# Kernel optimization log

Hardware: AMD Instinct MI355X
Metric: run time of the kernel (lower is better)

The kernel has to match this reference:

```python
import jax, jax.numpy as jnp
import numpy as np

N_OBJ, N_SR, N_V, N_F = 8192, 4096, 4100, 4096
EPS = 1e-8


def setup_inputs() -> dict:
    key = jax.random.key(0)
    k1, k2, k3, k4, k5 = jax.random.split(key, 5)
    obj_points = jax.random.normal(k1, (N_OBJ, 3), jnp.float32)
    sr_points = 0.5 * jax.random.normal(k2, (N_SR, 3), jnp.float32)
    hand_verts = 0.5 * jax.random.normal(k3, (N_V, 3), jnp.float32)
    face_normals = jax.random.normal(k4, (N_F, 3), jnp.float32)
    hand_faces = jax.random.randint(k5, (N_F, 3), 0, N_V)
    return dict(obj_points=obj_points, sr_points=sr_points,
                hand_verts=hand_verts, face_normals=face_normals,
                hand_faces=hand_faces)


def reference(obj_points, sr_points, hand_verts, face_normals, hand_faces):
    # --- get_NN: brute-force nearest hand point for every object point ---
    d2 = (jnp.sum(obj_points**2, -1)[:, None]
          + jnp.sum(sr_points**2, -1)[None, :]
          - 2.0 * obj_points @ sr_points.T)          # [N, M] squared dists
    nn_idx = jnp.argmin(d2, axis=1)                   # [N]
    trg_pts = sr_points[nn_idx]                       # batched_index_select -> [N,3]
    D = trg_pts - obj_points                          # ray directions [N,3]

    # --- ray-triangle intersection (plane test + 3 edge half-plane tests) ---
    # All [F,N,3] intermediates are avoided via triple-product expansion:
    # every quantity reduces to einsums of per-face [F,3] with per-ray [N,3].
    tri = hand_verts[hand_faces]                      # [F,3,3]
    v0, v1, v2 = tri[:, 0], tri[:, 1], tri[:, 2]
    n = face_normals                                  # [F,3]

    denom = jnp.einsum('fk,nk->fn', n, D)             # D . n   [F,N]
    num = jnp.sum(v0 * n, -1)[:, None] - jnp.einsum('fk,nk->fn', n, obj_points)
    dmask = jnp.abs(denom) > EPS
    t = num / jnp.where(dmask, denom, 1.0)            # plane hit parameter [F,N]

    def edge_sign(va, vb):
        # ((vb-va) x (P-va)) . n  with  P = O + t*D, expanded bilinearly
        c = jnp.cross(n, vb - va)                     # [F,3]
        base = (jnp.einsum('fk,nk->fn', c, obj_points)
                - jnp.sum(va * c, -1)[:, None])
        return base + t * jnp.einsum('fk,nk->fn', c, D)

    inside = ((edge_sign(v0, v1) >= 0)
              & (edge_sign(v1, v2) >= 0)
              & (edge_sign(v2, v0) >= 0))
    hit = inside & dmask & (t > EPS)                  # [F,N]

    hit_number = jnp.sum(hit.astype(jnp.int32), axis=0)   # per ray [N]
    interior = (hit_number % 2) != 0                        # odd parity -> inside

    diff = trg_pts - obj_points
    pen_dist = jnp.sqrt(jnp.sum(diff**2 * interior[:, None].astype(diff.dtype)) + 1e-12)

    # --- contact_map_of_m_to_n(obj_points, sr_points) ---
    nn_dist = jnp.sqrt(jnp.maximum(jnp.min(d2, axis=1), 0.0))
    cmap = 1.0 - 2.0 * (jax.nn.sigmoid(100.0 * nn_dist) - 0.5)

    return pen_dist, cmap
```

## Files before the change

### kernel.cpp

```cpp
#include <hip/hip_runtime.h>
#include <math.h>

#define N_OBJ 8192
#define N_SR  4096
#define N_F   4096
#define EPSF  1e-8f

typedef float v2f __attribute__((ext_vector_type(2)));
static __device__ __forceinline__ v2f sp(float x) { v2f r; r.x = x; r.y = x; return r; }
static __device__ __forceinline__ v2f vfma(v2f a, v2f b, v2f c) { return __builtin_elementwise_fma(a, b, c); }
static __device__ __forceinline__ v2f vmin2(v2f a, v2f b) { return __builtin_elementwise_min(a, b); }

__global__ void __launch_bounds__(256) nn_all(const float* __restrict__ obj,
                                              const float* __restrict__ sr,
                                              const float* __restrict__ hv,
                                              const float* __restrict__ fn,
                                              const int* __restrict__ hf,
                                              float* __restrict__ out,
                                              float4* __restrict__ Dws,
                                              int* __restrict__ hits,
                                              float4* __restrict__ F) {
    __shared__ float sx[N_SR], sy[N_SR], sz[N_SR];
    __shared__ float2 red[4][32];
    const int tid = threadIdx.x, b = blockIdx.x;

#pragma unroll
    for (int it = 0; it < 16; ++it) {
        int idx = it * 256 + tid;
        sx[idx] = sr[3 * idx];
        sy[idx] = sr[3 * idx + 1];
        sz[idx] = sr[3 * idx + 2];
    }
    if (tid < 32) hits[b * 32 + tid] = 0;
    if (tid < 16) {
        const int f = b * 16 + tid;
        const int i0 = hf[3*f], i1 = hf[3*f+1], i2 = hf[3*f+2];
        const float v0x = hv[3*i0], v0y = hv[3*i0+1], v0z = hv[3*i0+2];
        const float v1x = hv[3*i1], v1y = hv[3*i1+1], v1z = hv[3*i1+2];
        const float v2x = hv[3*i2], v2y = hv[3*i2+1], v2z = hv[3*i2+2];
        const float nx = fn[3*f], ny = fn[3*f+1], nz = fn[3*f+2];
        F[4*f+0] = make_float4(nx, ny, nz, v0x*nx + v0y*ny + v0z*nz);
        {
            float ex = v1x-v0x, ey = v1y-v0y, ez = v1z-v0z;
            float cx = ny*ez-nz*ey, cy = nz*ex-nx*ez, cz = nx*ey-ny*ex;
            F[4*f+1] = make_float4(cx, cy, cz, v0x*cx + v0y*cy + v0z*cz);
        }
        {
            float ex = v2x-v1x, ey = v2y-v1y, ez = v2z-v1z;
            float cx = ny*ez-nz*ey, cy = nz*ex-nx*ez, cz = nx*ey-ny*ex;
            F[4*f+2] = make_float4(cx, cy, cz, v1x*cx + v1y*cy + v1z*cz);
        }
        {
            float ex = v0x-v2x, ey = v0y-v2y, ez = v0z-v2z;
            float cx = ny*ez-nz*ey, cy = nz*ex-nx*ez, cz = nx*ey-ny*ex;
            F[4*f+3] = make_float4(cx, cy, cz, v2x*cx + v2y*cy + v2z*cz);
        }
    }
    __syncthreads();

    const int w = tid >> 6, lane = tid & 63;
    const int pp = lane >> 3, sl = lane & 7;
    const int s = w * 8 + sl;
    const int pbase = b * 32 + pp * 4;

    float ox[4], oy[4], oz[4];
#pragma unroll
    for (int k = 0; k < 4; ++k) {
        int p = pbase + k;
        ox[k] = obj[3*p]; oy[k] = obj[3*p+1]; oz[k] = obj[3*p+2];
    }
    float bd[4]; int bj[4];
#pragma unroll
    for (int k = 0; k < 4; ++k) { bd[k] = INFINITY; bj[k] = 0; }

#pragma unroll 4
    for (int j = 0; j < 128; ++j) {
        int e = j * 32 + s;
        float vx = sx[e], vy = sy[e], vz = sz[e];
#pragma unroll
        for (int k = 0; k < 4; ++k) {
            float dx = vx - ox[k], dy = vy - oy[k], dz = vz - oz[k];
            float d2 = fmaf(dx, dx, fmaf(dy, dy, dz * dz));
            if (d2 < bd[k]) { bd[k] = d2; bj[k] = j; }
        }
    }
    int bi[4];
#pragma unroll
    for (int k = 0; k < 4; ++k) bi[k] = bj[k] * 32 + s;
#pragma unroll
    for (int off = 4; off; off >>= 1) {
#pragma unroll
        for (int k = 0; k < 4; ++k) {
            float d = __shfl_down(bd[k], off, 8);
            int   i = __shfl_down(bi[k], off, 8);
            if (d < bd[k] || (d == bd[k] && i < bi[k])) { bd[k] = d; bi[k] = i; }
        }
    }
    if (sl == 0) {
#pragma unroll
        for (int k = 0; k < 4; ++k)
            red[w][pp * 4 + k] = make_float2(bd[k], __int_as_float(bi[k]));
    }
    __syncthreads();
    if (tid < 32) {
        float2 e0 = red[0][tid];
        float bdf = e0.x; int bif = __float_as_int(e0.y);
#pragma unroll
        for (int w2 = 1; w2 < 4; ++w2) {
            float2 e2 = red[w2][tid];
            float d = e2.x; int i = __float_as_int(e2.y);
            if (d < bdf || (d == bdf && i < bif)) { bdf = d; bif = i; }
        }
        int p = b * 32 + tid;
        float pox = obj[3*p], poy = obj[3*p+1], poz = obj[3*p+2];
        float dx = sx[bif] - pox, dy = sy[bif] - poy, dz = sz[bif] - poz;
        Dws[p] = make_float4(dx, dy, dz, dx*dx + dy*dy + dz*dz);
        float nn = sqrtf(fmaxf(bdf, 0.f));
        float sig = 1.f / (1.f + expf(-100.f * nn));
        out[1 + p] = 1.f - 2.f * (sig - 0.5f);
    }
}

#define RFC 64
__global__ void __launch_bounds__(256) ray_count(const float* __restrict__ obj,
                                                 const float4* __restrict__ Dws,
                                                 const float4* __restrict__ F,
                                                 int* __restrict__ hits) {
    __shared__ float4 sF[RFC * 4];
    const int tid = threadIdx.x;
    const int pg = blockIdx.x & 3, fc = blockIdx.x >> 2;
    {
        const float* Ff = (const float*)(F + (size_t)fc * RFC * 4);
        float* sf = (float*)sF;
#pragma unroll
        for (int i = 0; i < RFC * 16 / 256; ++i)
            sf[i * 256 + tid] = Ff[i * 256 + tid];
    }
    __syncthreads();

    v2f px[4], py[4], pz[4], qx[4], qy[4], qz[4];
    int cnt[8];
#pragma unroll
    for (int g = 0; g < 4; ++g) {
#pragma unroll
        for (int h = 0; h < 2; ++h) {
            int p = pg * 2048 + (g * 2 + h) * 256 + tid;
            px[g][h] = obj[3*p]; py[g][h] = obj[3*p+1]; pz[g][h] = obj[3*p+2];
            float4 D = Dws[p];
            qx[g][h] = D.x; qy[g][h] = D.y; qz[g][h] = D.z;
            cnt[g * 2 + h] = 0;
        }
    }

#pragma unroll 2
    for (int f = 0; f < RFC; ++f) {
        const float4 Fn = sF[4*f+0];
        const float4 C1 = sF[4*f+1];
        const float4 C2 = sF[4*f+2];
        const float4 C3 = sF[4*f+3];
#pragma unroll
        for (int g = 0; g < 4; ++g) {
            v2f denom = vfma(sp(Fn.z), qz[g], vfma(sp(Fn.y), qy[g], sp(Fn.x) * qx[g]));
            v2f num   = sp(Fn.w) - vfma(sp(Fn.z), pz[g], vfma(sp(Fn.y), py[g], sp(Fn.x) * px[g]));
            v2f dn = __builtin_elementwise_abs(denom);
            v2f nm = __builtin_elementwise_copysign(num, num * denom);
            v2f wx = vfma(px[g], dn, nm * qx[g]);
            v2f wy = vfma(py[g], dn, nm * qy[g]);
            v2f wz = vfma(pz[g], dn, nm * qz[g]);
            v2f q1 = vfma(sp(-C1.w), dn, vfma(sp(C1.z), wz, vfma(sp(C1.y), wy, sp(C1.x) * wx)));
            v2f q2 = vfma(sp(-C2.w), dn, vfma(sp(C2.z), wz, vfma(sp(C2.y), wy, sp(C2.x) * wx)));
            v2f q3 = vfma(sp(-C3.w), dn, vfma(sp(C3.z), wz, vfma(sp(C3.y), wy, sp(C3.x) * wx)));
            v2f mm = vmin2(q1, vmin2(q2, q3));
            mm = vmin2(mm, vfma(sp(-EPSF), dn, nm));
            mm = vmin2(mm, dn - sp(EPSF));
            cnt[g * 2 + 0] += (mm[0] >= 0.f) ? 1 : 0;
            cnt[g * 2 + 1] += (mm[1] >= 0.f) ? 1 : 0;
        }
    }
#pragma unroll
    for (int g = 0; g < 4; ++g) {
        atomicAdd(&hits[pg * 2048 + (g * 2 + 0) * 256 + tid], cnt[g * 2 + 0]);
        atomicAdd(&hits[pg * 2048 + (g * 2 + 1) * 256 + tid], cnt[g * 2 + 1]);
    }
}

__global__ void __launch_bounds__(256) finalize(const float4* __restrict__ Dws,
                                                const int* __restrict__ hits,
                                                float* __restrict__ out) {
    __shared__ float wsum[4];
    const int tid = threadIdx.x;
    float s = 0.f;
#pragma unroll 8
    for (int k = tid; k < N_OBJ; k += 256) {
        if (hits[k] & 1) s += Dws[k].w;
    }
#pragma unroll
    for (int off = 32; off > 0; off >>= 1) s += __shfl_down(s, off);
    if ((tid & 63) == 0) wsum[tid >> 6] = s;
    __syncthreads();
    if (tid == 0) {
        out[0] = sqrtf(wsum[0] + wsum[1] + wsum[2] + wsum[3] + 1e-12f);
    }
}

extern "C" void kernel_launch(void* const* d_in, const int* in_sizes, int n_in,
                              void* d_out, int out_size, void* d_ws, size_t ws_size,
                              hipStream_t stream) {
    const float* obj = (const float*)d_in[0];
    const float* sr  = (const float*)d_in[1];
    const float* hv  = (const float*)d_in[2];
    const float* fn  = (const float*)d_in[3];
    const int*   hf  = (const int*)d_in[4];
    float* out = (float*)d_out;

    char* ws = (char*)d_ws;
    float4* Dws  = (float4*)(ws + 0);
    int*    hits = (int*)  (ws + 131072);
    float4* F    = (float4*)(ws + 163840);

    nn_all<<<N_OBJ / 32, 256, 0, stream>>>(obj, sr, hv, fn, hf, out, Dws, hits, F);
    ray_count<<<256, 256, 0, stream>>>(obj, Dws, F, hits);
    finalize<<<1, 256, 0, stream>>>(Dws, hits, out);
}
```

Baseline: 120.4 us.

## Rework NN search with norm expansion, fuse finalize into ray kernel, rebalance grids

The nearest-neighbour kernel now precomputes squared norms of the hand points into packed shared-memory arrays. It computes distances as |s|^2 - 2 o·s with two-wide vector FMAs and reduces across a full wavefront instead of 8-lane groups plus a shared-memory stage, and it uses 512 blocks of 16 points. The ray kernel uses smaller face chunks over 512 blocks, issues its point loads before the face staging, and folds the final parity sum into the last block via an atomic completion counter, which drops the third launch. The expanded-distance form can change argmin tie and rounding behaviour relative to the direct difference form, and the last-block pattern relies on fences and atomics.

```diff
diff --git a/kernel.cpp b/kernel.cpp
--- a/kernel.cpp
+++ b/kernel.cpp
@@ -19,21 +19,27 @@
                                               float* __restrict__ out,
                                               float4* __restrict__ Dws,
                                               int* __restrict__ hits,
-                                              float4* __restrict__ F) {
-    __shared__ float sx[N_SR], sy[N_SR], sz[N_SR];
-    __shared__ float2 red[4][32];
+                                              float4* __restrict__ F,
+                                              int* __restrict__ done) {
+    __shared__ float4 pXY[N_SR / 2];
+    __shared__ float4 pZS[N_SR / 2];
     const int tid = threadIdx.x, b = blockIdx.x;
 
-#pragma unroll
-    for (int it = 0; it < 16; ++it) {
-        int idx = it * 256 + tid;
-        sx[idx] = sr[3 * idx];
-        sy[idx] = sr[3 * idx + 1];
-        sz[idx] = sr[3 * idx + 2];
-    }
-    if (tid < 32) hits[b * 32 + tid] = 0;
-    if (tid < 16) {
-        const int f = b * 16 + tid;
+    const float2* sr2 = (const float2*)sr;
+#pragma unroll
+    for (int i = 0; i < 8; ++i) {
+        int e = i * 256 + tid;
+        float2 A = sr2[3 * e], B = sr2[3 * e + 1], C = sr2[3 * e + 2];
+        float x0 = A.x, y0 = A.y, z0 = B.x, x1 = B.y, y1 = C.x, z1 = C.y;
+        float s0 = fmaf(x0, x0, fmaf(y0, y0, z0 * z0));
+        float s1 = fmaf(x1, x1, fmaf(y1, y1, z1 * z1));
+        pXY[e] = make_float4(x0, x1, y0, y1);
+        pZS[e] = make_float4(z0, z1, s0, s1);
+    }
+    if (tid < 16) hits[b * 16 + tid] = 0;
+    if (b == 0 && tid == 0) done[0] = 0;
+    if (tid < 8) {
+        const int f = b * 8 + tid;
         const int i0 = hf[3*f], i1 = hf[3*f+1], i2 = hf[3*f+2];
         const float v0x = hv[3*i0], v0y = hv[3*i0+1], v0z = hv[3*i0+2];
         const float v1x = hv[3*i1], v1y = hv[3*i1+1], v1z = hv[3*i1+2];
@@ -59,84 +65,80 @@
     __syncthreads();
 
     const int w = tid >> 6, lane = tid & 63;
-    const int pp = lane >> 3, sl = lane & 7;
-    const int s = w * 8 + sl;
-    const int pbase = b * 32 + pp * 4;
-
-    float ox[4], oy[4], oz[4];
+    const int pbase = b * 16 + w * 4;
+
+    float ox[4], oy[4], oz[4], aa[4];
 #pragma unroll
     for (int k = 0; k < 4; ++k) {
         int p = pbase + k;
         ox[k] = obj[3*p]; oy[k] = obj[3*p+1]; oz[k] = obj[3*p+2];
-    }
-    float bd[4]; int bj[4];
-#pragma unroll
-    for (int k = 0; k < 4; ++k) { bd[k] = INFINITY; bj[k] = 0; }
-
+        aa[k] = fmaf(ox[k], ox[k], fmaf(oy[k], oy[k], oz[k] * oz[k]));
+    }
+    float b0[4], b1[4]; int i0[4], i1[4];
+#pragma unroll
+    for (int k = 0; k < 4; ++k) { b0[k] = b1[k] = INFINITY; i0[k] = 0; i1[k] = 1; }
+
+    int e2 = lane * 2;
 #pragma unroll 4
-    for (int j = 0; j < 128; ++j) {
-        int e = j * 32 + s;
-        float vx = sx[e], vy = sy[e], vz = sz[e];
+    for (int step = 0; step < 32; ++step) {
+        int e = step * 64 + lane;
+        float4 A = pXY[e];
+        float4 B = pZS[e];
+        v2f X; X.x = A.x; X.y = A.y;
+        v2f Y; Y.x = A.z; Y.y = A.w;
+        v2f Z; Z.x = B.x; Z.y = B.y;
+        v2f SS; SS.x = B.z; SS.y = B.w;
 #pragma unroll
         for (int k = 0; k < 4; ++k) {
-            float dx = vx - ox[k], dy = vy - oy[k], dz = vz - oz[k];
-            float d2 = fmaf(dx, dx, fmaf(dy, dy, dz * dz));
-            if (d2 < bd[k]) { bd[k] = d2; bj[k] = j; }
-        }
-    }
-    int bi[4];
-#pragma unroll
-    for (int k = 0; k < 4; ++k) bi[k] = bj[k] * 32 + s;
-#pragma unroll
-    for (int off = 4; off; off >>= 1) {
-#pragma unroll
-        for (int k = 0; k < 4; ++k) {
-            float d = __shfl_down(bd[k], off, 8);
-            int   i = __shfl_down(bi[k], off, 8);
-            if (d < bd[k] || (d == bd[k] && i < bi[k])) { bd[k] = d; bi[k] = i; }
-        }
-    }
-    if (sl == 0) {
-#pragma unroll
-        for (int k = 0; k < 4; ++k)
-            red[w][pp * 4 + k] = make_float2(bd[k], __int_as_float(bi[k]));
-    }
-    __syncthreads();
-    if (tid < 32) {
-        float2 e0 = red[0][tid];
-        float bdf = e0.x; int bif = __float_as_int(e0.y);
-#pragma unroll
-        for (int w2 = 1; w2 < 4; ++w2) {
-            float2 e2 = red[w2][tid];
-            float d = e2.x; int i = __float_as_int(e2.y);
-            if (d < bdf || (d == bdf && i < bif)) { bdf = d; bif = i; }
-        }
-        int p = b * 32 + tid;
-        float pox = obj[3*p], poy = obj[3*p+1], poz = obj[3*p+2];
-        float dx = sx[bif] - pox, dy = sy[bif] - poy, dz = sz[bif] - poz;
-        Dws[p] = make_float4(dx, dy, dz, dx*dx + dy*dy + dz*dz);
-        float nn = sqrtf(fmaxf(bdf, 0.f));
-        float sig = 1.f / (1.f + expf(-100.f * nn));
-        out[1 + p] = 1.f - 2.f * (sig - 0.5f);
+            v2f d  = vfma(Z, sp(oz[k]), vfma(Y, sp(oy[k]), X * sp(ox[k])));
+            v2f d2 = vfma(d, sp(-2.f), SS);
+            bool c0 = d2.x < b0[k];
+            bool c1 = d2.y < b1[k];
+            b0[k] = c0 ? d2.x : b0[k];  i0[k] = c0 ? e2     : i0[k];
+            b1[k] = c1 ? d2.y : b1[k];  i1[k] = c1 ? e2 + 1 : i1[k];
+        }
+        e2 += 128;
+    }
+#pragma unroll
+    for (int k = 0; k < 4; ++k) {
+        float bd = b0[k]; int bi = i0[k];
+        if (b1[k] < bd || (b1[k] == bd && i1[k] < bi)) { bd = b1[k]; bi = i1[k]; }
+#pragma unroll
+        for (int off = 32; off > 0; off >>= 1) {
+            float d = __shfl_down(bd, off);
+            int   i = __shfl_down(bi, off);
+            if (d < bd || (d == bd && i < bi)) { bd = d; bi = i; }
+        }
+        if (lane == 0) {
+            int p = pbase + k;
+            float4 A = pXY[bi >> 1];
+            float4 B = pZS[bi >> 1];
+            int h = bi & 1;
+            float sx = h ? A.y : A.x;
+            float sy = h ? A.w : A.z;
+            float sz = h ? B.y : B.x;
+            float dx = sx - ox[k], dy = sy - oy[k], dz = sz - oz[k];
+            Dws[p] = make_float4(dx, dy, dz, fmaf(dx, dx, fmaf(dy, dy, dz * dz)));
+            float nn  = sqrtf(fmaxf(bd + aa[k], 0.f));
+            float sig = 1.f / (1.f + expf(-100.f * nn));
+            out[1 + p] = 1.f - 2.f * (sig - 0.5f);
+        }
     }
 }
 
-#define RFC 64
+#define RFC 32
+#define RAY_NB 512
 __global__ void __launch_bounds__(256) ray_count(const float* __restrict__ obj,
                                                  const float4* __restrict__ Dws,
                                                  const float4* __restrict__ F,
-                                                 int* __restrict__ hits) {
+                                                 int* __restrict__ hits,
+                                                 int* __restrict__ done,
+                                                 float* __restrict__ out) {
     __shared__ float4 sF[RFC * 4];
+    __shared__ float wsum[4];
+    __shared__ int lastf;
     const int tid = threadIdx.x;
     const int pg = blockIdx.x & 3, fc = blockIdx.x >> 2;
-    {
-        const float* Ff = (const float*)(F + (size_t)fc * RFC * 4);
-        float* sf = (float*)sF;
-#pragma unroll
-        for (int i = 0; i < RFC * 16 / 256; ++i)
-            sf[i * 256 + tid] = Ff[i * 256 + tid];
-    }
-    __syncthreads();
 
     v2f px[4], py[4], pz[4], qx[4], qy[4], qz[4];
     int cnt[8];
@@ -151,6 +153,14 @@
             cnt[g * 2 + h] = 0;
         }
     }
+    {
+        const float* Ff = (const float*)(F + (size_t)fc * RFC * 4);
+        float* sf = (float*)sF;
+#pragma unroll
+        for (int i = 0; i < RFC * 16 / 256; ++i)
+            sf[i * 256 + tid] = Ff[i * 256 + tid];
+    }
+    __syncthreads();
 
 #pragma unroll 2
     for (int f = 0; f < RFC; ++f) {
@@ -178,28 +188,28 @@
         }
     }
 #pragma unroll
-    for (int g = 0; g < 4; ++g) {
-        atomicAdd(&hits[pg * 2048 + (g * 2 + 0) * 256 + tid], cnt[g * 2 + 0]);
-        atomicAdd(&hits[pg * 2048 + (g * 2 + 1) * 256 + tid], cnt[g * 2 + 1]);
-    }
-}
-
-__global__ void __launch_bounds__(256) finalize(const float4* __restrict__ Dws,
-                                                const int* __restrict__ hits,
-                                                float* __restrict__ out) {
-    __shared__ float wsum[4];
-    const int tid = threadIdx.x;
-    float s = 0.f;
+    for (int g = 0; g < 8; ++g)
+        atomicAdd(&hits[pg * 2048 + g * 256 + tid], cnt[g]);
+
+    __syncthreads();
+    if (tid == 0) {
+        __threadfence();
+        lastf = (atomicAdd(done, 1) == RAY_NB - 1) ? 1 : 0;
+    }
+    __syncthreads();
+    if (lastf) {
+        float s = 0.f;
 #pragma unroll 8
-    for (int k = tid; k < N_OBJ; k += 256) {
-        if (hits[k] & 1) s += Dws[k].w;
-    }
-#pragma unroll
-    for (int off = 32; off > 0; off >>= 1) s += __shfl_down(s, off);
-    if ((tid & 63) == 0) wsum[tid >> 6] = s;
-    __syncthreads();
-    if (tid == 0) {
-        out[0] = sqrtf(wsum[0] + wsum[1] + wsum[2] + wsum[3] + 1e-12f);
+        for (int k = tid; k < N_OBJ; k += 256) {
+            int h = atomicAdd(&hits[k], 0);
+            if (h & 1) s += Dws[k].w;
+        }
+#pragma unroll
+        for (int off = 32; off > 0; off >>= 1) s += __shfl_down(s, off);
+        if ((tid & 63) == 0) wsum[tid >> 6] = s;
+        __syncthreads();
+        if (tid == 0)
+            out[0] = sqrtf(wsum[0] + wsum[1] + wsum[2] + wsum[3] + 1e-12f);
     }
 }
 
@@ -217,8 +227,8 @@
     float4* Dws  = (float4*)(ws + 0);
     int*    hits = (int*)  (ws + 131072);
     float4* F    = (float4*)(ws + 163840);
-
-    nn_all<<<N_OBJ / 32, 256, 0, stream>>>(obj, sr, hv, fn, hf, out, Dws, hits, F);
-    ray_count<<<256, 256, 0, stream>>>(obj, Dws, F, hits);
-    finalize<<<1, 256, 0, stream>>>(Dws, hits, out);
+    int*    done = (int*)  (ws + 425984);
+
+    nn_all<<<512, 256, 0, stream>>>(obj, sr, hv, fn, hf, out, Dws, hits, F, done);
+    ray_count<<<RAY_NB, 256, 0, stream>>>(obj, Dws, F, hits, done, out);
 }
```

New measurement: 115.4 us. 1.04x faster.
